# Performance work log

Measured on AMD Instinct MI355X. Metric: run time of the kernel, lower is better.

## Reference

```python
import jax, jax.numpy as jnp
import numpy as np

# static architecture constants
NUM_GRAPHS = 64
NODES_PER_GRAPH = 512
N_TOTAL = NUM_GRAPHS * NODES_PER_GRAPH          # 32768
AVG_DEG = 16
E_TOTAL = N_TOTAL * AVG_DEG                      # 524288
NODE_NUMBER = 1000
EMB = 128
DIMF = 128
NUM_LAYERS = 4
K = 64
DIM_TARGET = 2
LATENT = NUM_LAYERS * DIMF + 1                   # 513


def setup_inputs() -> dict:
    key = jax.random.key(0)
    ks = jax.random.split(key, 16)
    # node ids
    x = jax.random.randint(ks[0], (N_TOTAL,), 0, NODE_NUMBER, dtype=jnp.int32)
    # edges confined within each graph
    epg = NODES_PER_GRAPH * AVG_DEG
    src_l = jax.random.randint(ks[1], (NUM_GRAPHS, epg), 0, NODES_PER_GRAPH, dtype=jnp.int32)
    dst_l = jax.random.randint(ks[2], (NUM_GRAPHS, epg), 0, NODES_PER_GRAPH, dtype=jnp.int32)
    off = (jnp.arange(NUM_GRAPHS, dtype=jnp.int32) * NODES_PER_GRAPH)[:, None]
    edge_index = jnp.stack([(src_l + off).reshape(-1), (dst_l + off).reshape(-1)])  # [2,E]
    batch = jnp.repeat(jnp.arange(NUM_GRAPHS, dtype=jnp.int32), NODES_PER_GRAPH)

    def lin(k, fi, fo):
        return jax.random.normal(k, (fi, fo), jnp.float32) / np.sqrt(fi)

    emb = jax.random.normal(ks[3], (NODE_NUMBER, EMB), jnp.float32)
    W_convs = jnp.stack([lin(jax.random.fold_in(ks[4], l), EMB if l == 0 else DIMF, DIMF)
                         for l in range(NUM_LAYERS)])            # [L,128,128]
    b_convs = jnp.zeros((NUM_LAYERS, DIMF), jnp.float32)
    W_last = lin(ks[5], DIMF, 1)
    b_last = jnp.zeros((1,), jnp.float32)
    conv1_w = jax.random.normal(ks[6], (16, 1, LATENT), jnp.float32) / np.sqrt(LATENT)
    conv1_b = jnp.zeros((16,), jnp.float32)
    conv2_w = jax.random.normal(ks[7], (32, 16, 5), jnp.float32) / np.sqrt(16 * 5)
    conv2_b = jnp.zeros((32,), jnp.float32)
    dd = (K - 2) // 2 + 1                      # 32
    in_dense = (dd - 5 + 1) * 32               # 896
    d1_w = lin(ks[8], in_dense, dd)
    d1_b = jnp.zeros((dd,), jnp.float32)
    d2_w = lin(ks[9], dd, DIM_TARGET)
    d2_b = jnp.zeros((DIM_TARGET,), jnp.float32)
    return dict(x=x, edge_index=edge_index, batch=batch, emb=emb,
                W_convs=W_convs, b_convs=b_convs, W_last=W_last, b_last=b_last,
                conv1_w=conv1_w, conv1_b=conv1_b, conv2_w=conv2_w, conv2_b=conv2_b,
                d1_w=d1_w, d1_b=d1_b, d2_w=d2_w, d2_b=d2_b)


def _gcn(h, W, b, src, dst, norm):
    # linear -> gather -> degree-normalize -> scatter-add (DGCNNConv with aggr='add')
    h = h @ W + b
    msg = h[src] * norm[:, None]
    return jax.ops.segment_sum(msg, dst, num_segments=N_TOTAL)


def reference(x, edge_index, batch, emb, W_convs, b_convs, W_last, b_last,
              conv1_w, conv1_b, conv2_w, conv2_b, d1_w, d1_b, d2_w, d2_b):
    loops = jnp.arange(N_TOTAL, dtype=edge_index.dtype)
    src = jnp.concatenate([edge_index[0], loops])
    dst = jnp.concatenate([edge_index[1], loops])
    # deg = degree(src); norm = deg^-1 gathered at dst (as in DGCNNConv.message)
    deg = jax.ops.segment_sum(jnp.ones_like(src, jnp.float32), src, num_segments=N_TOTAL)
    norm = (1.0 / deg)[dst]

    h = emb[x]                                           # [N,128]
    hidden = []
    for l in range(NUM_LAYERS):
        h = jnp.tanh(_gcn(h, W_convs[l], b_convs[l], src, dst, norm))
        hidden.append(h)
    h = jnp.tanh(_gcn(h, W_last, b_last, src, dst, norm))  # [N,1]
    hidden.append(h)
    xcat = jnp.concatenate(hidden, axis=1)               # [N, 513]

    # global_sort_pool: batch is sorted with equal-size graphs -> dense reshape
    x3 = xcat.reshape(NUM_GRAPHS, NODES_PER_GRAPH, LATENT)
    order = jnp.argsort(-x3[..., -1], axis=1)[:, :K]     # descending by last channel, top-k
    pooled = jnp.take_along_axis(x3, order[:, :, None], axis=1)  # [B,K,513]

    # conv1d(1,16,kernel=513,stride=513) over [B,1,K*513] == per-row projection
    y1 = jax.nn.relu(jnp.einsum('bkd,od->bok', pooled, conv1_w[:, 0, :])
                     + conv1_b[None, :, None])           # [B,16,K]
    L = K // 2
    y1 = y1.reshape(NUM_GRAPHS, 16, L, 2).max(axis=-1)   # maxpool(2,2)
    y2 = jax.lax.conv_general_dilated(y1, conv2_w, (1,), 'VALID',
                                      dimension_numbers=('NCH', 'OIH', 'NCH'))
    y2 = jax.nn.relu(y2 + conv2_b[None, :, None])        # [B,32,L-4]
    flat = y2.reshape(NUM_GRAPHS, -1)                    # [B,896]
    h1 = jax.nn.relu(flat @ d1_w + d1_b)                 # dropout is identity in eval
    logits = h1 @ d2_w + d2_b
    return jax.nn.softmax(logits, axis=-1)
```

## Files before the change

kernel.cpp:

```cpp
#include <hip/hip_runtime.h>
#include <hip/hip_bf16.h>
#include <math.h>

#define N_TOTAL 32768
#define E_TOTAL 524288
#define NUM_GRAPHS 64
#define NPG 512
#define MAXD 64
#define KTOP 64
#define LATENT 513
#define PPAD 524

typedef __attribute__((ext_vector_type(8))) short bf16x8;
typedef __attribute__((ext_vector_type(4))) float f32x4;

__device__ __forceinline__ unsigned short f2bf(float f) {
    unsigned u = __float_as_uint(f);
    return (unsigned short)((u + 0x7FFFu + ((u >> 16) & 1u)) >> 16);
}
__device__ __forceinline__ float bf2f(unsigned short h) {
    return __uint_as_float(((unsigned)h) << 16);
}
__device__ __forceinline__ int swz(int bir, int row) {
    return (bir & ~127) | ((bir & 127) ^ ((row & 7) << 4));
}


__global__ __launch_bounds__(256) void k_init(int* __restrict__ deg, int* __restrict__ cnt) {
    int i = blockIdx.x * 256 + threadIdx.x;
    if (i < N_TOTAL) { deg[i] = 1; cnt[i] = 0; }
}

__global__ __launch_bounds__(256) void k_zero(int4* __restrict__ p) {
    p[(size_t)blockIdx.x * 256 + threadIdx.x] = make_int4(0, 0, 0, 0);
}

__global__ __launch_bounds__(256) void k_build(const int* __restrict__ ei,
                                               int* __restrict__ deg, int* __restrict__ cnt,
                                               int* __restrict__ adj, unsigned* __restrict__ Au) {
    int e = blockIdx.x * 256 + threadIdx.x;
    if (e >= E_TOTAL) return;
    int s = ei[e];
    int d = ei[E_TOTAL + e];
    atomicAdd(&deg[s], 1);
    int slot = atomicAdd(&cnt[d], 1);
    if (slot < MAXD) adj[(size_t)d * MAXD + slot] = s;
    int g = d >> 9, v = d & 511, u = s & 511;
    size_t bidx = ((size_t)(g * 512 + v) << 9) + u;
    atomicAdd(&Au[bidx >> 2], 1u << ((u & 3) << 3));
}

__global__ __launch_bounds__(256) void k_convA(const unsigned* __restrict__ Au,
                                               unsigned short* __restrict__ Asw) {
    size_t idx = (size_t)blockIdx.x * 256 + threadIdx.x;
    int g = (int)(idx >> 15);
    int rem = (int)(idx & 32767);
    int v = rem >> 6;
    int u0 = (rem & 63) * 8;
    size_t ebase = ((size_t)(g * 512 + v) << 9) + u0;
    uint2 cw = *(const uint2*)(Au + (ebase >> 2));
    unsigned r[4];
#pragma unroll
    for (int i = 0; i < 4; ++i) {
        unsigned wv = (i < 2) ? cw.x : cw.y;
        int sh = (i & 1) * 16;
        int ua = u0 + 2 * i, ub = ua + 1;
        float ca = (float)((wv >> sh) & 0xFFu)       + ((ua == v) ? 1.f : 0.f);
        float cb = (float)((wv >> (sh + 8)) & 0xFFu) + ((ub == v) ? 1.f : 0.f);
        r[i] = (unsigned)f2bf(ca) | ((unsigned)f2bf(cb) << 16);
    }
    *(int4*)(Asw + ebase) = make_int4(r[0], r[1], r[2], r[3]);
}

__global__ __launch_bounds__(256) void k_prep(const float* __restrict__ Wc,
                                              unsigned short* __restrict__ Wth,
                                              unsigned short* __restrict__ Wtl) {
    __shared__ float tile[64][65];
    int b = blockIdx.x;
    int l = b >> 2, t = b & 3;
    int k0 = (t >> 1) * 64, o0 = (t & 1) * 64;
    int lane = threadIdx.x & 63, q = threadIdx.x >> 6;
    const float* Wsrc = Wc + (size_t)l * 16384;
#pragma unroll
    for (int it = 0; it < 16; ++it) {
        int r = it * 4 + q;
        tile[r][lane] = Wsrc[(size_t)(k0 + r) * 128 + o0 + lane];
    }
    __syncthreads();
#pragma unroll
    for (int it = 0; it < 16; ++it) {
        int o = it * 4 + q;
        float v = tile[lane][o];
        unsigned short h = f2bf(v);
        unsigned short lo = f2bf(v - bf2f(h));
        size_t dst = (size_t)l * 16384 + (size_t)(o0 + o) * 128 + k0 + lane;
        Wth[dst] = h; Wtl[dst] = lo;
    }
}

__global__ __launch_bounds__(256) void k_embT(const int* __restrict__ x,
                                              const float* __restrict__ emb,
                                              unsigned short* __restrict__ Ph,
                                              unsigned short* __restrict__ Pl) {
    __shared__ float P[64][132];
    __shared__ int nodes[64];
    int b = blockIdx.x;
    int g = b >> 3, ck = b & 7;
    int tid = threadIdx.x;
    if (tid < 64) nodes[tid] = x[g * NPG + ck * 64 + tid];
    __syncthreads();
#pragma unroll
    for (int c = 0; c < 8; ++c) {
        int idx = tid + c * 256;
        int row = idx >> 5, c4 = idx & 31;
        float4 vv = *(const float4*)(emb + (size_t)nodes[row] * 128 + c4 * 4);
        *(float4*)&P[row][c4 * 4] = vv;
    }
    __syncthreads();
#pragma unroll
    for (int c = 0; c < 4; ++c) {
        int idx = tid + c * 256;
        int ch = idx >> 3, grp = idx & 7;
        unsigned hw[4], lw[4];
#pragma unroll
        for (int j = 0; j < 4; ++j) {
            float a  = P[grp * 8 + 2 * j][ch];
            float bq = P[grp * 8 + 2 * j + 1][ch];
            unsigned short ha = f2bf(a),  hb = f2bf(bq);
            unsigned short la = f2bf(a - bf2f(ha)), lb = f2bf(bq - bf2f(hb));
            hw[j] = (unsigned)ha | ((unsigned)hb << 16);
            lw[j] = (unsigned)la | ((unsigned)lb << 16);
        }
        size_t base = ((size_t)g * 128 + ch) * 512 + ck * 64 + grp * 8;
        *(int4*)(Ph + base) = make_int4(hw[0], hw[1], hw[2], hw[3]);
        *(int4*)(Pl + base) = make_int4(lw[0], lw[1], lw[2], lw[3]);
    }
}


__global__ __launch_bounds__(256) void k_layer(const unsigned short* __restrict__ Ph,
                                               const unsigned short* __restrict__ Pl,
                                               const unsigned short* __restrict__ Asw,
                                               const unsigned short* __restrict__ Wth,
                                               const unsigned short* __restrict__ Wtl,
                                               const float* __restrict__ bvec,
                                               const float* __restrict__ Wl,
                                               const float* __restrict__ bl,
                                               float* __restrict__ tmp,
                                               float* __restrict__ Hout,
                                               unsigned short* __restrict__ Poh,
                                               unsigned short* __restrict__ Pol,
                                               const int* __restrict__ cnt,
                                               const int* __restrict__ deg) {
    __shared__ char lds[65536];
    int tid = threadIdx.x;
    int w = tid >> 6, lane = tid & 63;
    int bid = blockIdx.x;
    int g = (bid & 7) * 8 + ((bid >> 3) & 7);
    int vblk = bid >> 6;
    int nodebase = g * NPG + vblk * 64;
    int rowbase = nodebase + w * 16;
    int r = lane & 15, kb = lane >> 4;

    const unsigned short* Pgh = Ph + (size_t)g * 128 * 512;
    const unsigned short* Pgl = Pl + (size_t)g * 128 * 512;
    const unsigned short* Arow = Asw + (size_t)(rowbase + r) * 512;

#define STAGE(buf, kt)                                                                     \
    {                                                                                      \
        _Pragma("unroll")                                                                  \
        for (int c = 0; c < 8; ++c) {                                                      \
            int sb = c * 256 + w * 64;                         \
            int slot = sb + lane;                                                          \
            int arr = slot >> 10;                                                          \
            int j = slot & 1023;                                                           \
            int row = j >> 3, off16 = j & 7;                                               \
            const unsigned short* src = (arr ? Pgl : Pgh)                                  \
                + (size_t)row * 512 + (kt) * 64 + ((off16 ^ (row & 7)) << 3);              \
            char* dst = lds + (buf) * 32768 + sb * 16;   \
            __builtin_amdgcn_global_load_lds((const unsigned*)src, (unsigned*)dst,         \
                                             16, 0, 0);                                    \
        }                                                                                  \
    }

    f32x4 acc[8];
#pragma unroll
    for (int n = 0; n < 8; ++n) acc[n] = (f32x4){0.f, 0.f, 0.f, 0.f};

    STAGE(0, 0);
    __syncthreads();
    int cbuf = 0;
    for (int kt = 0; kt < 8; ++kt) {
        if (kt < 7) STAGE(cbuf ^ 1, kt + 1);
        const char* cur = lds + cbuf * 32768;
#pragma unroll
        for (int s2 = 0; s2 < 2; ++s2) {
            bf16x8 aA = *(const bf16x8*)(Arow + kt * 64 + s2 * 32 + kb * 8);
#pragma unroll
            for (int n = 0; n < 8; ++n) {
                int ch = n * 16 + r;
                int u = s2 * 4 + kb;
                int boff = ch * 128 + ((u ^ (ch & 7)) << 4);
                bf16x8 bh  = *(const bf16x8*)(cur + boff);
                bf16x8 bl2 = *(const bf16x8*)(cur + 16384 + boff);
                acc[n] = __builtin_amdgcn_mfma_f32_16x16x32_bf16(aA, bh,  acc[n], 0, 0, 0);
                acc[n] = __builtin_amdgcn_mfma_f32_16x16x32_bf16(aA, bl2, acc[n], 0, 0, 0);
            }
        }
        __syncthreads();
        cbuf ^= 1;
    }
#undef STAGE

#pragma unroll
    for (int n = 0; n < 8; ++n) {
#pragma unroll
        for (int q = 0; q < 4; ++q) {
            int v64 = w * 16 + kb * 4 + q;
            int ch = n * 16 + r;
            float s = acc[n][q];
            unsigned short h = f2bf(s), lo = f2bf(s - bf2f(h));
            int addr = v64 * 256 + swz(ch * 2, v64);
            *(unsigned short*)(lds + addr)         = h;
            *(unsigned short*)(lds + 16384 + addr) = lo;
        }
    }
    __syncthreads();

    bf16x8 ah[4], al[4];
#pragma unroll
    for (int ks = 0; ks < 4; ++ks) {
        int v64 = w * 16 + r;
        int addr = v64 * 256 + swz(ks * 64 + kb * 16, v64);
        ah[ks] = *(const bf16x8*)(lds + addr);
        al[ks] = *(const bf16x8*)(lds + 16384 + addr);
    }
    float invd[4], cp1[4];
#pragma unroll
    for (int q = 0; q < 4; ++q) {
        int nd = rowbase + kb * 4 + q;
        invd[q] = 1.0f / (float)deg[nd];
        cp1[q]  = (float)(cnt[nd] + 1);
    }
    float z[4] = {0.f, 0.f, 0.f, 0.f};
    unsigned hiW[8][2], loW[8][2];
#pragma unroll
    for (int ct = 0; ct < 8; ++ct) {
        const unsigned short* Wh = Wth + (size_t)(ct * 16 + r) * 128;
        const unsigned short* Wo = Wtl + (size_t)(ct * 16 + r) * 128;
        f32x4 a = {0.f, 0.f, 0.f, 0.f};
#pragma unroll
        for (int ks = 0; ks < 4; ++ks) {
            bf16x8 wh = *(const bf16x8*)(Wh + ks * 32 + kb * 8);
            bf16x8 wl = *(const bf16x8*)(Wo + ks * 32 + kb * 8);
            a = __builtin_amdgcn_mfma_f32_16x16x32_bf16(ah[ks], wh, a, 0, 0, 0);
            a = __builtin_amdgcn_mfma_f32_16x16x32_bf16(ah[ks], wl, a, 0, 0, 0);
            a = __builtin_amdgcn_mfma_f32_16x16x32_bf16(al[ks], wh, a, 0, 0, 0);
        }
        float bcol = bvec[ct * 16 + r];
        float wlast = Wl ? Wl[ct * 16 + r] : 0.f;
        unsigned short hq[4], lq[4];
#pragma unroll
        for (int q = 0; q < 4; ++q) {
            float val = tanhf((a[q] + bcol * cp1[q]) * invd[q]);
            Hout[(size_t)(rowbase + kb * 4 + q) * 128 + ct * 16 + r] = val;
            z[q] = fmaf(val, wlast, z[q]);
            hq[q] = f2bf(val);
            lq[q] = f2bf(val - bf2f(hq[q]));
        }
        hiW[ct][0] = (unsigned)hq[0] | ((unsigned)hq[1] << 16);
        hiW[ct][1] = (unsigned)hq[2] | ((unsigned)hq[3] << 16);
        loW[ct][0] = (unsigned)lq[0] | ((unsigned)lq[1] << 16);
        loW[ct][1] = (unsigned)lq[2] | ((unsigned)lq[3] << 16);
    }

    if (Poh) {
        __syncthreads();
#pragma unroll
        for (int ct = 0; ct < 8; ++ct) {
            int o = ct * 16 + r;
            int v64 = w * 16 + kb * 4;
            int addr = o * 128 + swz(v64 * 2, o);
            *(int2*)(lds + addr)         = make_int2(hiW[ct][0], hiW[ct][1]);
            *(int2*)(lds + 16384 + addr) = make_int2(loW[ct][0], loW[ct][1]);
        }
        __syncthreads();
#pragma unroll
        for (int c = 0; c < 8; ++c) {
            int idx = tid + c * 256;
            int arr = idx >> 10;
            int j = idx & 1023;
            int o = j >> 3, off16 = j & 7;
            int4 v = *(const int4*)(lds + arr * 16384 + o * 128 + swz(off16 * 16, o));
            unsigned short* dst = (arr ? Pol : Poh) + ((size_t)g * 128 + o) * 512 + vblk * 64 + off16 * 8;
            *(int4*)dst = v;
        }
    }

    if (Wl) {
#pragma unroll
        for (int m = 1; m < 16; m <<= 1) {
            z[0] += __shfl_xor(z[0], m); z[1] += __shfl_xor(z[1], m);
            z[2] += __shfl_xor(z[2], m); z[3] += __shfl_xor(z[3], m);
        }
        if (r == 0) {
            float b0 = bl[0];
#pragma unroll
            for (int q = 0; q < 4; ++q) tmp[rowbase + kb * 4 + q] = z[q] + b0;
        }
    }
}


__global__ __launch_bounds__(256) void k_sort(const float* __restrict__ tmp,
                                              const int* __restrict__ adj,
                                              const int* __restrict__ cnt,
                                              const int* __restrict__ deg,
                                              float* __restrict__ lastc,
                                              int* __restrict__ topk) {
    __shared__ float v[512];
    __shared__ int ix[512];
    int g = blockIdx.x, tid = threadIdx.x;
    for (int i = tid; i < 512; i += 256) {
        int node = g * NPG + i;
        float s = tmp[node];
        int c = cnt[node]; if (c > MAXD) c = MAXD;
        const int* av = adj + (size_t)node * MAXD;
#pragma unroll 4
        for (int q = 0; q < c; ++q) s += tmp[av[q]];
        float val = tanhf(s / (float)deg[node]);
        lastc[node] = val;
        v[i] = val; ix[i] = i;
    }
    __syncthreads();
    for (int ksz = 2; ksz <= 512; ksz <<= 1) {
        for (int jj = ksz >> 1; jj > 0; jj >>= 1) {
            for (int i = tid; i < 512; i += 256) {
                int p = i ^ jj;
                if (p > i) {
                    float va = v[i], vb = v[p];
                    int ia = ix[i], ib = ix[p];
                    bool b_before_a = (vb > va) || (vb == va && ib < ia);
                    bool up = (i & ksz) == 0;
                    bool sw = up ? b_before_a : !b_before_a;
                    if (sw) { v[i] = vb; v[p] = va; ix[i] = ib; ix[p] = ia; }
                }
            }
            __syncthreads();
        }
    }
    for (int k = tid; k < KTOP; k += 256) topk[g * KTOP + k] = g * NPG + ix[k];
}


__global__ __launch_bounds__(256) void k_conv1(const int* __restrict__ topk,
                                               const float* __restrict__ h0,
                                               const float* __restrict__ h1,
                                               const float* __restrict__ h2,
                                               const float* __restrict__ h3,
                                               const float* __restrict__ lastc,
                                               const float* __restrict__ c1w,
                                               const float* __restrict__ c1b,
                                               float* __restrict__ y1p) {
    __shared__ float P[16][PPAD];
    __shared__ float Y1c[16][16];
    __shared__ int nodes[16];
    int bid = blockIdx.x;
    int g = bid >> 2, cc = bid & 3;
    int tid = threadIdx.x;
    if (tid < 16) nodes[tid] = topk[g * KTOP + cc * 16 + tid];
    __syncthreads();
    {
        int r = tid >> 4, t4 = tid & 15;
        int node = nodes[r];
#pragma unroll
        for (int jj = 0; jj < 8; ++jj) {
            int d = (t4 + 16 * jj) * 4;
            const float* src = (d < 128) ? h0 : (d < 256) ? h1 : (d < 384) ? h2 : h3;
            float4 val = *(const float4*)(src + (size_t)node * 128 + (d & 127));
            *(float4*)&P[r][d] = val;
        }
        if (t4 == 0) P[r][512] = lastc[node];
    }
    __syncthreads();
    int o = tid >> 4, kk = tid & 15;
    const float* w = c1w + (size_t)o * LATENT;
    float a0 = 0.f, a1 = 0.f, a2 = 0.f, a3 = 0.f;
    for (int d = 0; d < 512; d += 4) {
        float4 p = *(const float4*)&P[kk][d];
        a0 = fmaf(p.x, w[d],     a0);
        a1 = fmaf(p.y, w[d + 1], a1);
        a2 = fmaf(p.z, w[d + 2], a2);
        a3 = fmaf(p.w, w[d + 3], a3);
    }
    float s = ((a0 + a1) + (a2 + a3)) + P[kk][512] * w[512] + c1b[o];
    Y1c[o][kk] = fmaxf(s, 0.f);
    __syncthreads();
    if (tid < 128) {
        int oo = tid >> 3, l = tid & 7;
        y1p[(size_t)g * 512 + oo * 32 + cc * 8 + l] = fmaxf(Y1c[oo][2 * l], Y1c[oo][2 * l + 1]);
    }
}


__global__ __launch_bounds__(256) void k_tail(const float* __restrict__ y1p,
                                              const float* __restrict__ c2w, const float* __restrict__ c2b,
                                              const float* __restrict__ d1w, const float* __restrict__ d1b,
                                              const float* __restrict__ d2w, const float* __restrict__ d2b,
                                              float* __restrict__ out) {
    __shared__ float Y1P[16][32];
    __shared__ float Y2[32][28];
    __shared__ float H1s[32];
    __shared__ float red[256];
    int g = blockIdx.x, tid = threadIdx.x;
    for (int t = tid; t < 512; t += 256) ((float*)Y1P)[t] = y1p[(size_t)g * 512 + t];
    __syncthreads();
    for (int t = tid; t < 32 * 28; t += 256) {
        int o2 = t / 28, tt = t - o2 * 28;
        float s = c2b[o2];
#pragma unroll
        for (int i = 0; i < 16; ++i)
#pragma unroll
            for (int dt = 0; dt < 5; ++dt)
                s = fmaf(Y1P[i][tt + dt], c2w[o2 * 80 + i * 5 + dt], s);
        Y2[o2][tt] = fmaxf(s, 0.f);
    }
    __syncthreads();
    {
        int jcol = tid >> 3, part = tid & 7;
        float s = 0.f;
        for (int rr = 0; rr < 4; ++rr) {
            int o2 = part * 4 + rr;
            int base = o2 * 28;
            for (int tt = 0; tt < 28; ++tt)
                s = fmaf(Y2[o2][tt], d1w[(size_t)(base + tt) * 32 + jcol], s);
        }
        red[tid] = s;
        __syncthreads();
        if (part == 0) {
            float t = 0.f;
#pragma unroll
            for (int p = 0; p < 8; ++p) t += red[tid + p];
            H1s[jcol] = fmaxf(t + d1b[jcol], 0.f);
        }
        __syncthreads();
    }
    if (tid == 0) {
        float l0 = d2b[0], l1 = d2b[1];
        for (int jc = 0; jc < 32; ++jc) {
            l0 = fmaf(H1s[jc], d2w[jc * 2 + 0], l0);
            l1 = fmaf(H1s[jc], d2w[jc * 2 + 1], l1);
        }
        float m = fmaxf(l0, l1);
        float e0 = expf(l0 - m), e1 = expf(l1 - m);
        float inv = 1.f / (e0 + e1);
        out[g * 2 + 0] = e0 * inv;
        out[g * 2 + 1] = e1 * inv;
    }
}


extern "C" void kernel_launch(void* const* d_in, const int* in_sizes, int n_in,
                              void* d_out, int out_size, void* d_ws, size_t ws_size,
                              hipStream_t stream) {
    const int*   x    = (const int*)d_in[0];
    const int*   ei   = (const int*)d_in[1];
    const float* emb  = (const float*)d_in[3];
    const float* Wc   = (const float*)d_in[4];
    const float* bc   = (const float*)d_in[5];
    const float* Wl   = (const float*)d_in[6];
    const float* bl   = (const float*)d_in[7];
    const float* c1w  = (const float*)d_in[8];
    const float* c1b  = (const float*)d_in[9];
    const float* c2w  = (const float*)d_in[10];
    const float* c2b  = (const float*)d_in[11];
    const float* d1w  = (const float*)d_in[12];
    const float* d1b  = (const float*)d_in[13];
    const float* d2w  = (const float*)d_in[14];
    const float* d2b  = (const float*)d_in[15];
    float* out = (float*)d_out;

    char* ws = (char*)d_ws;
    int*   deg  = (int*)ws;            ws += (size_t)N_TOTAL * 4;
    int*   cnt  = (int*)ws;            ws += (size_t)N_TOTAL * 4;
    int*   adj  = (int*)ws;            ws += (size_t)N_TOTAL * MAXD * 4;
    float* Hid0 = (float*)ws;          ws += (size_t)N_TOTAL * 128 * 4;
    float* Hid1 = (float*)ws;          ws += (size_t)N_TOTAL * 128 * 4;
    float* Hid2 = (float*)ws;          ws += (size_t)N_TOTAL * 128 * 4;
    float* Hid3 = (float*)ws;          ws += (size_t)N_TOTAL * 128 * 4;
    unsigned short* Wth = (unsigned short*)ws;  ws += (size_t)4 * 128 * 128 * 2;
    unsigned short* Wtl = (unsigned short*)ws;  ws += (size_t)4 * 128 * 128 * 2;
    float* tmp  = (float*)ws;          ws += (size_t)N_TOTAL * 4;
    float* lastc= (float*)ws;          ws += (size_t)N_TOTAL * 4;
    int*   topk = (int*)ws;            ws += (size_t)NUM_GRAPHS * KTOP * 4;
    float* y1p  = (float*)ws;          ws += (size_t)NUM_GRAPHS * 16 * 32 * 4;
    unsigned* Au = (unsigned*)ws;      ws += (size_t)NUM_GRAPHS * 512 * 512;
    unsigned short* Asw = (unsigned short*)ws;  ws += (size_t)NUM_GRAPHS * 512 * 512 * 2;
    unsigned short* PAh = (unsigned short*)ws;  ws += (size_t)NUM_GRAPHS * 128 * 512 * 2;
    unsigned short* PAl = (unsigned short*)ws;  ws += (size_t)NUM_GRAPHS * 128 * 512 * 2;
    unsigned short* PBh = (unsigned short*)ws;  ws += (size_t)NUM_GRAPHS * 128 * 512 * 2;
    unsigned short* PBl = (unsigned short*)ws;  ws += (size_t)NUM_GRAPHS * 128 * 512 * 2;

    k_init <<<N_TOTAL / 256, 256, 0, stream>>>(deg, cnt);
    k_zero <<<4096, 256, 0, stream>>>((int4*)Au);
    k_build<<<E_TOTAL / 256, 256, 0, stream>>>(ei, deg, cnt, adj, Au);
    k_prep <<<16, 256, 0, stream>>>(Wc, Wth, Wtl);
    k_convA<<<8192, 256, 0, stream>>>(Au, Asw);
    k_embT <<<NUM_GRAPHS * 8, 256, 0, stream>>>(x, emb, PAh, PAl);

    float* Hids[4] = {Hid0, Hid1, Hid2, Hid3};
    unsigned short* Pin_h[4] = {PAh, PBh, PAh, PBh};
    unsigned short* Pin_l[4] = {PAl, PBl, PAl, PBl};
    unsigned short* Pout_h[4] = {PBh, PAh, PBh, nullptr};
    unsigned short* Pout_l[4] = {PBl, PAl, PBl, nullptr};
    for (int l = 0; l < 4; ++l) {
        const float* wl  = (l == 3) ? Wl : nullptr;
        const float* blp = (l == 3) ? bl : nullptr;
        float*       tp  = (l == 3) ? tmp : nullptr;
        k_layer<<<512, 256, 0, stream>>>(Pin_h[l], Pin_l[l], Asw,
                                         Wth + (size_t)l * 16384, Wtl + (size_t)l * 16384,
                                         bc + (size_t)l * 128, wl, blp, tp,
                                         Hids[l], Pout_h[l], Pout_l[l], cnt, deg);
    }
    k_sort <<<NUM_GRAPHS, 256, 0, stream>>>(tmp, adj, cnt, deg, lastc, topk);
    k_conv1<<<NUM_GRAPHS * 4, 256, 0, stream>>>(topk, Hid0, Hid1, Hid2, Hid3, lastc, c1w, c1b, y1p);
    k_tail <<<NUM_GRAPHS, 256, 0, stream>>>(y1p, c2w, c2b, d1w, d1b, d2w, d2b, out);
}
```

Measured before the change: 332.6 us.

## Build dense adjacency in LDS per graph slice and drop adjacency lists

Replaces the global byte-count atomics, the zeroing pass and the conversion pass with one kernel per graph slice that histograms edges in shared memory and writes the bf16 adjacency directly. The padded adjacency list is removed, and the final scalar aggregation becomes a separate dense row-dot kernel over the bf16 adjacency instead of gathering neighbours inside the sort kernel. This is meant to cut global atomic traffic and large workspace reads and writes. The cost is that each block rescans all edges of its graph (8x redundant reads), and there is one extra kernel launch.

```diff
diff --git a/kernel.cpp b/kernel.cpp
--- a/kernel.cpp
+++ b/kernel.cpp
@@ -6,7 +6,6 @@
 #define E_TOTAL 524288
 #define NUM_GRAPHS 64
 #define NPG 512
-#define MAXD 64
 #define KTOP 64
 #define LATENT 513
 #define PPAD 524
@@ -31,45 +30,53 @@
     if (i < N_TOTAL) { deg[i] = 1; cnt[i] = 0; }
 }
 
-__global__ __launch_bounds__(256) void k_zero(int4* __restrict__ p) {
-    p[(size_t)blockIdx.x * 256 + threadIdx.x] = make_int4(0, 0, 0, 0);
-}
-
 __global__ __launch_bounds__(256) void k_build(const int* __restrict__ ei,
-                                               int* __restrict__ deg, int* __restrict__ cnt,
-                                               int* __restrict__ adj, unsigned* __restrict__ Au) {
+                                               int* __restrict__ deg, int* __restrict__ cnt) {
     int e = blockIdx.x * 256 + threadIdx.x;
     if (e >= E_TOTAL) return;
-    int s = ei[e];
-    int d = ei[E_TOTAL + e];
-    atomicAdd(&deg[s], 1);
-    int slot = atomicAdd(&cnt[d], 1);
-    if (slot < MAXD) adj[(size_t)d * MAXD + slot] = s;
-    int g = d >> 9, v = d & 511, u = s & 511;
-    size_t bidx = ((size_t)(g * 512 + v) << 9) + u;
-    atomicAdd(&Au[bidx >> 2], 1u << ((u & 3) << 3));
-}
-
-__global__ __launch_bounds__(256) void k_convA(const unsigned* __restrict__ Au,
-                                               unsigned short* __restrict__ Asw) {
-    size_t idx = (size_t)blockIdx.x * 256 + threadIdx.x;
-    int g = (int)(idx >> 15);
-    int rem = (int)(idx & 32767);
-    int v = rem >> 6;
-    int u0 = (rem & 63) * 8;
-    size_t ebase = ((size_t)(g * 512 + v) << 9) + u0;
-    uint2 cw = *(const uint2*)(Au + (ebase >> 2));
-    unsigned r[4];
-#pragma unroll
-    for (int i = 0; i < 4; ++i) {
-        unsigned wv = (i < 2) ? cw.x : cw.y;
-        int sh = (i & 1) * 16;
-        int ua = u0 + 2 * i, ub = ua + 1;
-        float ca = (float)((wv >> sh) & 0xFFu)       + ((ua == v) ? 1.f : 0.f);
-        float cb = (float)((wv >> (sh + 8)) & 0xFFu) + ((ub == v) ? 1.f : 0.f);
-        r[i] = (unsigned)f2bf(ca) | ((unsigned)f2bf(cb) << 16);
-    }
-    *(int4*)(Asw + ebase) = make_int4(r[0], r[1], r[2], r[3]);
+    atomicAdd(&deg[ei[e]], 1);
+    atomicAdd(&cnt[ei[E_TOTAL + e]], 1);
+}
+
+__global__ __launch_bounds__(256) void k_buildA(const int* __restrict__ ei,
+                                                unsigned short* __restrict__ Asw) {
+    __shared__ unsigned Acnt[8192];
+    int bid = blockIdx.x;
+    int g = bid >> 3, sl = bid & 7;
+    int v0 = sl * 64;
+    int tid = threadIdx.x;
+#pragma unroll
+    for (int i = 0; i < 32; ++i) Acnt[tid + i * 256] = 0;
+    __syncthreads();
+    const int* srcp = ei + (size_t)g * 8192;
+    const int* dstp = ei + E_TOTAL + (size_t)g * 8192;
+    for (int i = 0; i < 32; ++i) {
+        int e = tid + i * 256;
+        int d = dstp[e] & 511;
+        int s = srcp[e] & 511;
+        if (d >= v0 && d < v0 + 64) {
+            int cell = (d - v0) * 512 + s;
+            atomicAdd(&Acnt[cell >> 2], 1u << ((cell & 3) << 3));
+        }
+    }
+    __syncthreads();
+#pragma unroll
+    for (int j = 0; j < 32; ++j) {
+        int wi = tid + j * 256;
+        unsigned wv = Acnt[wi];
+        int cell0 = wi * 4;
+        int row = cell0 >> 9, col0 = cell0 & 511;
+        int diag = v0 + row;
+        unsigned short b[4];
+#pragma unroll
+        for (int h = 0; h < 4; ++h) {
+            float c = (float)((wv >> (8 * h)) & 0xFFu) + ((col0 + h == diag) ? 1.f : 0.f);
+            b[h] = f2bf(c);
+        }
+        *(int2*)(Asw + ((size_t)(g * 512 + v0 + row) << 9) + col0) =
+            make_int2((unsigned)b[0] | ((unsigned)b[1] << 16),
+                      (unsigned)b[2] | ((unsigned)b[3] << 16));
+    }
 }
 
 __global__ __launch_bounds__(256) void k_prep(const float* __restrict__ Wc,
@@ -170,14 +177,14 @@
     {                                                                                      \
         _Pragma("unroll")                                                                  \
         for (int c = 0; c < 8; ++c) {                                                      \
-            int sb = c * 256 + w * 64;                         \
+            int sb = c * 256 + w * 64;                                                     \
             int slot = sb + lane;                                                          \
             int arr = slot >> 10;                                                          \
             int j = slot & 1023;                                                           \
             int row = j >> 3, off16 = j & 7;                                               \
             const unsigned short* src = (arr ? Pgl : Pgh)                                  \
                 + (size_t)row * 512 + (kt) * 64 + ((off16 ^ (row & 7)) << 3);              \
-            char* dst = lds + (buf) * 32768 + sb * 16;   \
+            char* dst = lds + (buf) * 32768 + sb * 16;                                     \
             __builtin_amdgcn_global_load_lds((const unsigned*)src, (unsigned*)dst,         \
                                              16, 0, 0);                                    \
         }                                                                                  \
@@ -312,26 +319,39 @@
 }
 
 
-__global__ __launch_bounds__(256) void k_sort(const float* __restrict__ tmp,
-                                              const int* __restrict__ adj,
-                                              const int* __restrict__ cnt,
-                                              const int* __restrict__ deg,
-                                              float* __restrict__ lastc,
+__global__ __launch_bounds__(256) void k_lastagg(const unsigned short* __restrict__ Asw,
+                                                 const float* __restrict__ tmp,
+                                                 const int* __restrict__ deg,
+                                                 float* __restrict__ lastc) {
+    __shared__ float t[512];
+    int bid = blockIdx.x;
+    int g = bid >> 3, sl = bid & 7;
+    int tid = threadIdx.x;
+    if (tid < 128) *(float4*)&t[tid * 4] = *(const float4*)(tmp + (size_t)g * 512 + tid * 4);
+    __syncthreads();
+    int row = tid >> 2, q = tid & 3;
+    int v = g * NPG + sl * 64 + row;
+    const unsigned short* Ar = Asw + ((size_t)v << 9) + q * 128;
+    float s = 0.f;
+#pragma unroll
+    for (int c = 0; c < 128; c += 8) {
+        bf16x8 a8 = *(const bf16x8*)(Ar + c);
+#pragma unroll
+        for (int h = 0; h < 8; ++h)
+            s = fmaf(bf2f((unsigned short)a8[h]), t[q * 128 + c + h], s);
+    }
+    s += __shfl_xor(s, 1);
+    s += __shfl_xor(s, 2);
+    if (q == 0) lastc[v] = tanhf(s / (float)deg[v]);
+}
+
+
+__global__ __launch_bounds__(256) void k_sort(const float* __restrict__ lastc,
                                               int* __restrict__ topk) {
     __shared__ float v[512];
     __shared__ int ix[512];
     int g = blockIdx.x, tid = threadIdx.x;
-    for (int i = tid; i < 512; i += 256) {
-        int node = g * NPG + i;
-        float s = tmp[node];
-        int c = cnt[node]; if (c > MAXD) c = MAXD;
-        const int* av = adj + (size_t)node * MAXD;
-#pragma unroll 4
-        for (int q = 0; q < c; ++q) s += tmp[av[q]];
-        float val = tanhf(s / (float)deg[node]);
-        lastc[node] = val;
-        v[i] = val; ix[i] = i;
-    }
+    for (int i = tid; i < 512; i += 256) { v[i] = lastc[g * NPG + i]; ix[i] = i; }
     __syncthreads();
     for (int ksz = 2; ksz <= 512; ksz <<= 1) {
         for (int jj = ksz >> 1; jj > 0; jj >>= 1) {
@@ -483,7 +503,6 @@
     char* ws = (char*)d_ws;
     int*   deg  = (int*)ws;            ws += (size_t)N_TOTAL * 4;
     int*   cnt  = (int*)ws;            ws += (size_t)N_TOTAL * 4;
-    int*   adj  = (int*)ws;            ws += (size_t)N_TOTAL * MAXD * 4;
     float* Hid0 = (float*)ws;          ws += (size_t)N_TOTAL * 128 * 4;
     float* Hid1 = (float*)ws;          ws += (size_t)N_TOTAL * 128 * 4;
     float* Hid2 = (float*)ws;          ws += (size_t)N_TOTAL * 128 * 4;
@@ -494,19 +513,17 @@
     float* lastc= (float*)ws;          ws += (size_t)N_TOTAL * 4;
     int*   topk = (int*)ws;            ws += (size_t)NUM_GRAPHS * KTOP * 4;
     float* y1p  = (float*)ws;          ws += (size_t)NUM_GRAPHS * 16 * 32 * 4;
-    unsigned* Au = (unsigned*)ws;      ws += (size_t)NUM_GRAPHS * 512 * 512;
     unsigned short* Asw = (unsigned short*)ws;  ws += (size_t)NUM_GRAPHS * 512 * 512 * 2;
     unsigned short* PAh = (unsigned short*)ws;  ws += (size_t)NUM_GRAPHS * 128 * 512 * 2;
     unsigned short* PAl = (unsigned short*)ws;  ws += (size_t)NUM_GRAPHS * 128 * 512 * 2;
     unsigned short* PBh = (unsigned short*)ws;  ws += (size_t)NUM_GRAPHS * 128 * 512 * 2;
     unsigned short* PBl = (unsigned short*)ws;  ws += (size_t)NUM_GRAPHS * 128 * 512 * 2;
 
-    k_init <<<N_TOTAL / 256, 256, 0, stream>>>(deg, cnt);
-    k_zero <<<4096, 256, 0, stream>>>((int4*)Au);
-    k_build<<<E_TOTAL / 256, 256, 0, stream>>>(ei, deg, cnt, adj, Au);
-    k_prep <<<16, 256, 0, stream>>>(Wc, Wth, Wtl);
-    k_convA<<<8192, 256, 0, stream>>>(Au, Asw);
-    k_embT <<<NUM_GRAPHS * 8, 256, 0, stream>>>(x, emb, PAh, PAl);
+    k_init  <<<N_TOTAL / 256, 256, 0, stream>>>(deg, cnt);
+    k_build <<<E_TOTAL / 256, 256, 0, stream>>>(ei, deg, cnt);
+    k_prep  <<<16, 256, 0, stream>>>(Wc, Wth, Wtl);
+    k_buildA<<<512, 256, 0, stream>>>(ei, Asw);
+    k_embT  <<<NUM_GRAPHS * 8, 256, 0, stream>>>(x, emb, PAh, PAl);
 
     float* Hids[4] = {Hid0, Hid1, Hid2, Hid3};
     unsigned short* Pin_h[4] = {PAh, PBh, PAh, PBh};
@@ -522,7 +539,8 @@
                                          bc + (size_t)l * 128, wl, blp, tp,
                                          Hids[l], Pout_h[l], Pout_l[l], cnt, deg);
     }
-    k_sort <<<NUM_GRAPHS, 256, 0, stream>>>(tmp, adj, cnt, deg, lastc, topk);
-    k_conv1<<<NUM_GRAPHS * 4, 256, 0, stream>>>(topk, Hid0, Hid1, Hid2, Hid3, lastc, c1w, c1b, y1p);
-    k_tail <<<NUM_GRAPHS, 256, 0, stream>>>(y1p, c2w, c2b, d1w, d1b, d2w, d2b, out);
-}
+    k_lastagg<<<512, 256, 0, stream>>>(Asw, tmp, deg, lastc);
+    k_sort   <<<NUM_GRAPHS, 256, 0, stream>>>(lastc, topk);
+    k_conv1  <<<NUM_GRAPHS * 4, 256, 0, stream>>>(topk, Hid0, Hid1, Hid2, Hid3, lastc, c1w, c1b, y1p);
+    k_tail   <<<NUM_GRAPHS, 256, 0, stream>>>(y1p, c2w, c2b, d1w, d1b, d2w, d2b, out);
+}
```

Result: no change. 327.0 us (-1.7%).
